# Kernel optimization log

Hardware: AMD Instinct MI355X
Metric: run time of the kernel (lower is better)

Reference implementation:

```python
import jax, jax.numpy as jnp
import numpy as np

NUM_ITER = 3
EPS = 1e-7


def squash(t, axis=-1):
    sq = jnp.sum(t * t, axis=axis, keepdims=True)
    safe_norm = jnp.sqrt(sq + EPS)
    return (sq / (1.0 + sq)) * (t / safe_norm)


def setup_inputs() -> dict:
    key = jax.random.key(0)
    k1, k2 = jax.random.split(key)
    B, D, P, O, I = 256, 10, 1152, 16, 8
    x = jax.random.normal(k1, (B, P, I), dtype=jnp.float32)
    W = 0.01 * jax.random.normal(k2, (1, D, P, O, I), dtype=jnp.float32)
    return {"x": x, "W": W}


def reference(x, W):
    B = x.shape[0]
    D, P = W.shape[1], W.shape[2]
    # u_hat: [B, D, P, O]  (W @ u with u = x[:,None,:, :,None])
    u_hat = jnp.einsum("zdpoi,bpi->bdpo", W, x)
    temp_u_hat = jax.lax.stop_gradient(u_hat)
    b = jnp.zeros((B, D, P, 1), dtype=u_hat.dtype)
    for _ in range(NUM_ITER - 1):
        c = jax.nn.softmax(b, axis=1)          # [B, D, P, 1]
        s = jnp.sum(c * temp_u_hat, axis=2)    # [B, D, O]
        v = squash(s)                          # [B, D, O]
        uv = jnp.einsum("bdpo,bdo->bdp", temp_u_hat, v)[..., None]
        b = b + uv
    c = jax.nn.softmax(b, axis=1)
    s = jnp.sum(c * u_hat, axis=2)
    return squash(s)  # [B, D, O]
```

## Files before the change

kernel.cpp:

```cpp
#include <hip/hip_runtime.h>

namespace {

constexpr int BATCH = 256;
constexpr int DCAPS = 10;
constexpr int PCAPS = 1152;
constexpr int ODIM  = 16;
constexpr int IDIM  = 8;
constexpr float EPS_ = 1e-7f;

constexpr int BT    = 64;
constexpr int NBB   = BATCH / BT;
constexpr int NPBLK = 128;
constexpr int PPB   = PCAPS / NPBLK;
constexpr int WAVES = 5;
constexpr int XSTR  = PPB * IDIM + 1;
constexpr int SDO   = BATCH * DCAPS * ODIM;

template <int NV>
__global__ __launch_bounds__(320, 4)
void route_kernel(const float* __restrict__ x, const float* __restrict__ W,
                  const float* __restrict__ v0, const float* __restrict__ v1,
                  float* __restrict__ part)
{
    const int tid  = threadIdx.x;
    const int lane = tid & 63;
    const int wid  = __builtin_amdgcn_readfirstlane(tid >> 6);
    const int d0   = 2 * wid;
    const int pBlk = blockIdx.x & (NPBLK - 1);
    const int bBlk = blockIdx.x >> 7;
    const int b    = bBlk * BT + lane;
    const int p0   = pBlk * PPB;

    __shared__ float xs[BT][XSTR];
    __shared__ float lx[DCAPS][BT];

    for (int k = tid; k < BT * PPB * 2; k += 320) {
        const int bl = k / (PPB * 2);
        const int j  = k - bl * (PPB * 2);
        const int pp = j >> 1;
        const int ih = (j & 1) * 4;
        const float4 w4 = reinterpret_cast<const float4*>(x)[
            ((size_t)(bBlk * BT + bl) * PCAPS + p0 + pp) * 2 + (j & 1)];
        float* dst = &xs[bl][pp * IDIM + ih];
        dst[0] = w4.x; dst[1] = w4.y; dst[2] = w4.z; dst[3] = w4.w;
    }
    __syncthreads();

    float vr[2][ODIM];
    if constexpr (NV >= 1) {
#pragma unroll
        for (int dd = 0; dd < 2; ++dd) {
            const float4* vp = reinterpret_cast<const float4*>(
                v0 + ((size_t)b * DCAPS + d0 + dd) * ODIM);
#pragma unroll
            for (int q = 0; q < 4; ++q) {
                float4 t = vp[q];
                if constexpr (NV == 2) {
                    const float4 u = reinterpret_cast<const float4*>(
                        v1 + ((size_t)b * DCAPS + d0 + dd) * ODIM)[q];
                    t.x += u.x; t.y += u.y; t.z += u.z; t.w += u.w;
                }
                vr[dd][q * 4 + 0] = t.x; vr[dd][q * 4 + 1] = t.y;
                vr[dd][q * 4 + 2] = t.z; vr[dd][q * 4 + 3] = t.w;
            }
        }
    }

    float s_acc[2][ODIM];
#pragma unroll
    for (int dd = 0; dd < 2; ++dd)
#pragma unroll
        for (int o = 0; o < ODIM; ++o) s_acc[dd][o] = 0.f;

    for (int pp = 0; pp < PPB; ++pp) {
        float xr[IDIM];
#pragma unroll
        for (int i = 0; i < IDIM; ++i) xr[i] = xs[lane][pp * IDIM + i];

        float uh[2][ODIM];
#pragma unroll
        for (int dd = 0; dd < 2; ++dd) {
            const float4* wp4 = reinterpret_cast<const float4*>(
                W + (((size_t)(d0 + dd) * PCAPS + p0 + pp) * ODIM) * IDIM);
#pragma unroll
            for (int o = 0; o < ODIM; ++o) {
                const float4 wa = wp4[o * 2 + 0];
                const float4 wb = wp4[o * 2 + 1];
                float acc;
                acc = wa.x * xr[0];
                acc = fmaf(wa.y, xr[1], acc);
                acc = fmaf(wa.z, xr[2], acc);
                acc = fmaf(wa.w, xr[3], acc);
                acc = fmaf(wb.x, xr[4], acc);
                acc = fmaf(wb.y, xr[5], acc);
                acc = fmaf(wb.z, xr[6], acc);
                acc = fmaf(wb.w, xr[7], acc);
                uh[dd][o] = acc;
            }
        }

        if constexpr (NV == 0) {
#pragma unroll
            for (int dd = 0; dd < 2; ++dd)
#pragma unroll
                for (int o = 0; o < ODIM; ++o)
                    s_acc[dd][o] = fmaf(0.1f, uh[dd][o], s_acc[dd][o]);
        } else {
            float l2[2];
#pragma unroll
            for (int dd = 0; dd < 2; ++dd) {
                float t = uh[dd][0] * vr[dd][0];
#pragma unroll
                for (int o = 1; o < ODIM; ++o) t = fmaf(uh[dd][o], vr[dd][o], t);
                l2[dd] = t;
            }
            lx[d0 + 0][lane] = l2[0];
            lx[d0 + 1][lane] = l2[1];
            __syncthreads();
            float lv[DCAPS];
#pragma unroll
            for (int d = 0; d < DCAPS; ++d) lv[d] = lx[d][lane];
            __syncthreads();
            float mx = lv[0];
#pragma unroll
            for (int d = 1; d < DCAPS; ++d) mx = fmaxf(mx, lv[d]);
            float den = 0.f;
#pragma unroll
            for (int d = 0; d < DCAPS; ++d) den += __expf(lv[d] - mx);
            const float inv = 1.0f / den;
#pragma unroll
            for (int dd = 0; dd < 2; ++dd) {
                const float c = __expf(l2[dd] - mx) * inv;
#pragma unroll
                for (int o = 0; o < ODIM; ++o)
                    s_acc[dd][o] = fmaf(c, uh[dd][o], s_acc[dd][o]);
            }
        }
    }

#pragma unroll
    for (int dd = 0; dd < 2; ++dd) {
        float* dst = part + ((((size_t)pBlk * NBB + bBlk) * DCAPS + d0 + dd) * BT
                             + lane) * ODIM;
#pragma unroll
        for (int q = 0; q < 4; ++q) {
            float4 t;
            t.x = s_acc[dd][q * 4 + 0]; t.y = s_acc[dd][q * 4 + 1];
            t.z = s_acc[dd][q * 4 + 2]; t.w = s_acc[dd][q * 4 + 3];
            reinterpret_cast<float4*>(dst)[q] = t;
        }
    }
}

__global__ __launch_bounds__(256)
void squash_kernel(const float* __restrict__ part, float* __restrict__ out)
{
    constexpr int CG  = 8;
    constexpr int CPC = NPBLK / CG;
    const int tid = threadIdx.x;
    const int cg  = tid >> 5;
    const int u   = tid & 31;
    const int gu  = blockIdx.x * 32 + u;
    const int b   = gu / DCAPS;
    const int d   = gu - b * DCAPS;
    const int bb  = b >> 6;
    const int bl  = b & 63;

    float4 a = make_float4(0, 0, 0, 0), b4 = a, c4 = a, d4 = a;
    for (int k = 0; k < CPC; ++k) {
        const int c = cg * CPC + k;
        const float4* sp = reinterpret_cast<const float4*>(
            part + ((((size_t)c * NBB + bb) * DCAPS + d) * BT + bl) * ODIM);
        float4 p0 = sp[0], p1 = sp[1], p2 = sp[2], p3 = sp[3];
        a.x += p0.x; a.y += p0.y; a.z += p0.z; a.w += p0.w;
        b4.x += p1.x; b4.y += p1.y; b4.z += p1.z; b4.w += p1.w;
        c4.x += p2.x; c4.y += p2.y; c4.z += p2.z; c4.w += p2.w;
        d4.x += p3.x; d4.y += p3.y; d4.z += p3.z; d4.w += p3.w;
    }

    __shared__ float red[CG][32][ODIM + 1];
    float* r = red[cg][u];
    r[0]  = a.x;  r[1]  = a.y;  r[2]  = a.z;  r[3]  = a.w;
    r[4]  = b4.x; r[5]  = b4.y; r[6]  = b4.z; r[7]  = b4.w;
    r[8]  = c4.x; r[9]  = c4.y; r[10] = c4.z; r[11] = c4.w;
    r[12] = d4.x; r[13] = d4.y; r[14] = d4.z; r[15] = d4.w;
    __syncthreads();

    if (cg == 0) {
        float s[ODIM];
#pragma unroll
        for (int e = 0; e < ODIM; ++e) s[e] = red[0][u][e];
#pragma unroll
        for (int c2 = 1; c2 < CG; ++c2)
#pragma unroll
            for (int e = 0; e < ODIM; ++e) s[e] += red[c2][u][e];

        float sq = 0.f;
#pragma unroll
        for (int e = 0; e < ODIM; ++e) sq = fmaf(s[e], s[e], sq);
        const float scale = (sq / (1.0f + sq)) / sqrtf(sq + EPS_);
#pragma unroll
        for (int e = 0; e < ODIM; ++e) out[(size_t)gu * ODIM + e] = s[e] * scale;
    }
}

}

extern "C" void kernel_launch(void* const* d_in, const int* in_sizes, int n_in,
                              void* d_out, int out_size, void* d_ws, size_t ws_size,
                              hipStream_t stream)
{
    const float* x = (const float*)d_in[0];
    const float* W = (const float*)d_in[1];
    float* out = (float*)d_out;

    float* v0   = (float*)d_ws;
    float* v1   = v0 + SDO;
    float* part = v1 + SDO;

    const dim3 rblk(320);
    const dim3 rgrid(NPBLK * NBB);
    const dim3 sblk(256);
    const dim3 sgrid(BATCH * DCAPS / 32);

    route_kernel<0><<<rgrid, rblk, 0, stream>>>(x, W, nullptr, nullptr, part);
    squash_kernel<<<sgrid, sblk, 0, stream>>>(part, v0);

    route_kernel<1><<<rgrid, rblk, 0, stream>>>(x, W, v0, nullptr, part);
    squash_kernel<<<sgrid, sblk, 0, stream>>>(part, v1);

    route_kernel<2><<<rgrid, rblk, 0, stream>>>(x, W, v0, v1, part);
    squash_kernel<<<sgrid, sblk, 0, stream>>>(part, out);
}
```

Before: 199.5 us.

## Stage W tile in LDS, templatize P-chunk size, restructure squash reduction

The route kernel now copies the block's W slice for all ten output capsules into shared memory before the compute loop. Inner-loop weight reads then hit LDS instead of global/L1, which was previously re-read per wave. The P-chunk size becomes a template parameter and uses 6 when the workspace is large enough (more blocks, more partials), else 9. The squash kernel is rewritten so each capsule is handled by 32 threads with float4 lanes, giving more parallelism, at the cost of extra syncs and more partials to reduce.

```diff
diff --git a/kernel.cpp b/kernel.cpp
--- a/kernel.cpp
+++ b/kernel.cpp
@@ -9,41 +9,51 @@
 constexpr int IDIM  = 8;
 constexpr float EPS_ = 1e-7f;
 
-constexpr int BT    = 64;
-constexpr int NBB   = BATCH / BT;
-constexpr int NPBLK = 128;
-constexpr int PPB   = PCAPS / NPBLK;
-constexpr int WAVES = 5;
-constexpr int XSTR  = PPB * IDIM + 1;
-constexpr int SDO   = BATCH * DCAPS * ODIM;
-
-template <int NV>
+constexpr int BT  = 64;
+constexpr int NBB = BATCH / BT;
+constexpr int SDO = BATCH * DCAPS * ODIM;
+
+template <int NV, int PPBt>
 __global__ __launch_bounds__(320, 4)
 void route_kernel(const float* __restrict__ x, const float* __restrict__ W,
                   const float* __restrict__ v0, const float* __restrict__ v1,
                   float* __restrict__ part)
 {
+    constexpr int NPBLK = PCAPS / PPBt;
+    constexpr int XSTR  = PPBt * IDIM + 1;
+    constexpr int WT4   = PPBt * DCAPS * ODIM * IDIM / 4;
+
     const int tid  = threadIdx.x;
     const int lane = tid & 63;
     const int wid  = __builtin_amdgcn_readfirstlane(tid >> 6);
     const int d0   = 2 * wid;
-    const int pBlk = blockIdx.x & (NPBLK - 1);
-    const int bBlk = blockIdx.x >> 7;
+    const int pBlk = blockIdx.x % NPBLK;
+    const int bBlk = blockIdx.x / NPBLK;
     const int b    = bBlk * BT + lane;
-    const int p0   = pBlk * PPB;
-
+    const int p0   = pBlk * PPBt;
+
+    __shared__ float wlds[PPBt * DCAPS * ODIM * IDIM];
     __shared__ float xs[BT][XSTR];
     __shared__ float lx[DCAPS][BT];
 
-    for (int k = tid; k < BT * PPB * 2; k += 320) {
-        const int bl = k / (PPB * 2);
-        const int j  = k - bl * (PPB * 2);
+    float4* wl4 = reinterpret_cast<float4*>(wlds);
+    const float4* W4 = reinterpret_cast<const float4*>(W);
+    for (int k = tid; k < WT4; k += 320) {
+        const int d   = k / (PPBt * 32);
+        const int rem = k - d * (PPBt * 32);
+        const int pp  = rem >> 5;
+        const int q   = rem & 31;
+        wl4[k] = W4[((size_t)d * PCAPS + p0 + pp) * 32 + q];
+    }
+    const float4* X4 = reinterpret_cast<const float4*>(x);
+    for (int k = tid; k < BT * PPBt * 2; k += 320) {
+        const int bl = k / (PPBt * 2);
+        const int j  = k - bl * (PPBt * 2);
         const int pp = j >> 1;
-        const int ih = (j & 1) * 4;
-        const float4 w4 = reinterpret_cast<const float4*>(x)[
-            ((size_t)(bBlk * BT + bl) * PCAPS + p0 + pp) * 2 + (j & 1)];
-        float* dst = &xs[bl][pp * IDIM + ih];
-        dst[0] = w4.x; dst[1] = w4.y; dst[2] = w4.z; dst[3] = w4.w;
+        const int h  = j & 1;
+        const float4 t = X4[((size_t)(bBlk * BT + bl) * PCAPS + p0 + pp) * 2 + h];
+        float* dst = &xs[bl][pp * IDIM + h * 4];
+        dst[0] = t.x; dst[1] = t.y; dst[2] = t.z; dst[3] = t.w;
     }
     __syncthreads();
 
@@ -73,7 +83,7 @@
 #pragma unroll
         for (int o = 0; o < ODIM; ++o) s_acc[dd][o] = 0.f;
 
-    for (int pp = 0; pp < PPB; ++pp) {
+    for (int pp = 0; pp < PPBt; ++pp) {
         float xr[IDIM];
 #pragma unroll
         for (int i = 0; i < IDIM; ++i) xr[i] = xs[lane][pp * IDIM + i];
@@ -81,12 +91,12 @@
         float uh[2][ODIM];
 #pragma unroll
         for (int dd = 0; dd < 2; ++dd) {
-            const float4* wp4 = reinterpret_cast<const float4*>(
-                W + (((size_t)(d0 + dd) * PCAPS + p0 + pp) * ODIM) * IDIM);
+            const float4* wv = reinterpret_cast<const float4*>(wlds)
+                               + ((size_t)(d0 + dd) * PPBt + pp) * 32;
 #pragma unroll
             for (int o = 0; o < ODIM; ++o) {
-                const float4 wa = wp4[o * 2 + 0];
-                const float4 wb = wp4[o * 2 + 1];
+                const float4 wa = wv[o * 2 + 0];
+                const float4 wb = wv[o * 2 + 1];
                 float acc;
                 acc = wa.x * xr[0];
                 acc = fmaf(wa.y, xr[1], acc);
@@ -153,56 +163,79 @@
     }
 }
 
+template <int NP>
 __global__ __launch_bounds__(256)
 void squash_kernel(const float* __restrict__ part, float* __restrict__ out)
 {
-    constexpr int CG  = 8;
-    constexpr int CPC = NPBLK / CG;
+    constexpr int CPC = NP / 8;
     const int tid = threadIdx.x;
-    const int cg  = tid >> 5;
-    const int u   = tid & 31;
-    const int gu  = blockIdx.x * 32 + u;
+    const int u   = tid >> 5;
+    const int l   = tid & 31;
+    const int cg  = l >> 2;
+    const int q   = l & 3;
+    const int gu  = blockIdx.x * 8 + u;
     const int b   = gu / DCAPS;
     const int d   = gu - b * DCAPS;
     const int bb  = b >> 6;
     const int bl  = b & 63;
 
-    float4 a = make_float4(0, 0, 0, 0), b4 = a, c4 = a, d4 = a;
+    float4 acc = make_float4(0, 0, 0, 0);
     for (int k = 0; k < CPC; ++k) {
         const int c = cg * CPC + k;
-        const float4* sp = reinterpret_cast<const float4*>(
-            part + ((((size_t)c * NBB + bb) * DCAPS + d) * BT + bl) * ODIM);
-        float4 p0 = sp[0], p1 = sp[1], p2 = sp[2], p3 = sp[3];
-        a.x += p0.x; a.y += p0.y; a.z += p0.z; a.w += p0.w;
-        b4.x += p1.x; b4.y += p1.y; b4.z += p1.z; b4.w += p1.w;
-        c4.x += p2.x; c4.y += p2.y; c4.z += p2.z; c4.w += p2.w;
-        d4.x += p3.x; d4.y += p3.y; d4.z += p3.z; d4.w += p3.w;
-    }
-
-    __shared__ float red[CG][32][ODIM + 1];
-    float* r = red[cg][u];
-    r[0]  = a.x;  r[1]  = a.y;  r[2]  = a.z;  r[3]  = a.w;
-    r[4]  = b4.x; r[5]  = b4.y; r[6]  = b4.z; r[7]  = b4.w;
-    r[8]  = c4.x; r[9]  = c4.y; r[10] = c4.z; r[11] = c4.w;
-    r[12] = d4.x; r[13] = d4.y; r[14] = d4.z; r[15] = d4.w;
+        const float4 p4 = reinterpret_cast<const float4*>(
+            part + ((((size_t)c * NBB + bb) * DCAPS + d) * BT + bl) * ODIM)[q];
+        acc.x += p4.x; acc.y += p4.y; acc.z += p4.z; acc.w += p4.w;
+    }
+
+    __shared__ float4 sred[8][8][4];
+    __shared__ float4 sfin[8][4];
+    __shared__ float  nrm[8][4];
+    __shared__ float  sscale[8];
+    sred[u][cg][q] = acc;
     __syncthreads();
 
     if (cg == 0) {
-        float s[ODIM];
-#pragma unroll
-        for (int e = 0; e < ODIM; ++e) s[e] = red[0][u][e];
-#pragma unroll
-        for (int c2 = 1; c2 < CG; ++c2)
-#pragma unroll
-            for (int e = 0; e < ODIM; ++e) s[e] += red[c2][u][e];
-
-        float sq = 0.f;
-#pragma unroll
-        for (int e = 0; e < ODIM; ++e) sq = fmaf(s[e], s[e], sq);
-        const float scale = (sq / (1.0f + sq)) / sqrtf(sq + EPS_);
-#pragma unroll
-        for (int e = 0; e < ODIM; ++e) out[(size_t)gu * ODIM + e] = s[e] * scale;
-    }
+        float4 s = sred[u][0][q];
+#pragma unroll
+        for (int c2 = 1; c2 < 8; ++c2) {
+            const float4 t = sred[u][c2][q];
+            s.x += t.x; s.y += t.y; s.z += t.z; s.w += t.w;
+        }
+        sfin[u][q] = s;
+        nrm[u][q]  = s.x * s.x + s.y * s.y + s.z * s.z + s.w * s.w;
+    }
+    __syncthreads();
+    if (l == 0) {
+        const float sq = nrm[u][0] + nrm[u][1] + nrm[u][2] + nrm[u][3];
+        sscale[u] = (sq / (1.0f + sq)) / sqrtf(sq + EPS_);
+    }
+    __syncthreads();
+    if (cg == 0) {
+        float4 s = sfin[u][q];
+        const float sc = sscale[u];
+        s.x *= sc; s.y *= sc; s.z *= sc; s.w *= sc;
+        reinterpret_cast<float4*>(out)[(size_t)gu * 4 + q] = s;
+    }
+}
+
+template <int PPBt>
+void run_all(const float* x, const float* W, float* v0, float* v1, float* part,
+             float* out, hipStream_t stream)
+{
+    constexpr int NPBLK = PCAPS / PPBt;
+    const dim3 rblk(320);
+    const dim3 rgrid(NPBLK * NBB);
+    const dim3 sblk(256);
+    const dim3 sgrid(BATCH * DCAPS / 8);
+
+    route_kernel<0, PPBt><<<rgrid, rblk, 0, stream>>>(x, W, nullptr, nullptr, part);
+    squash_kernel<NPBLK><<<sgrid, sblk, 0, stream>>>(part, v0);
+
+    route_kernel<1, PPBt><<<rgrid, rblk, 0, stream>>>(x, W, v0, nullptr, part);
+    squash_kernel<NPBLK><<<sgrid, sblk, 0, stream>>>(part, v1);
+
+    route_kernel<2, PPBt><<<rgrid, rblk, 0, stream>>>(x, W, v0, v1, part);
+    squash_kernel<NPBLK><<<sgrid, sblk, 0, stream>>>(part, out);
 }
 
 }
@@ -219,17 +252,10 @@
     float* v1   = v0 + SDO;
     float* part = v1 + SDO;
 
-    const dim3 rblk(320);
-    const dim3 rgrid(NPBLK * NBB);
-    const dim3 sblk(256);
-    const dim3 sgrid(BATCH * DCAPS / 32);
-
-    route_kernel<0><<<rgrid, rblk, 0, stream>>>(x, W, nullptr, nullptr, part);
-    squash_kernel<<<sgrid, sblk, 0, stream>>>(part, v0);
-
-    route_kernel<1><<<rgrid, rblk, 0, stream>>>(x, W, v0, nullptr, part);
-    squash_kernel<<<sgrid, sblk, 0, stream>>>(part, v1);
-
-    route_kernel<2><<<rgrid, rblk, 0, stream>>>(x, W, v0, v1, part);
-    squash_kernel<<<sgrid, sblk, 0, stream>>>(part, out);
-}
+    const size_t need6 = ((size_t)2 + 192) * SDO * sizeof(float);
+    if (ws_size >= need6) {
+        run_all<6>(x, W, v0, v1, part, out, stream);
+    } else {
+        run_all<9>(x, W, v0, v1, part, out, stream);
+    }
+}
```

Result: slower. 206.4 us (+3.4%).
